# Kernel optimization log

Measured on AMD Instinct MI355X. Metric: run time of the kernel, lower is better.

## Reference

```python
import jax, jax.numpy as jnp
import numpy as np

B, D_ENC, T = 4, 512, 256
D_PRED, U = 640, 128
H, V = 640, 1025  # joint_hidden, num_classes + blank


def setup_inputs() -> dict:
    key = jax.random.key(0)
    ks = jax.random.split(key, 8)
    s = lambda d: 1.0 / np.sqrt(d)
    return {
        "encoder_outputs": jax.random.normal(ks[0], (B, D_ENC, T), jnp.float32),
        "decoder_outputs": jax.random.normal(ks[1], (B, D_PRED, U), jnp.float32),
        "W_enc": jax.random.normal(ks[2], (H, D_ENC), jnp.float32) * s(D_ENC),
        "b_enc": jax.random.normal(ks[3], (H,), jnp.float32) * s(D_ENC),
        "W_pred": jax.random.normal(ks[4], (H, D_PRED), jnp.float32) * s(D_PRED),
        "b_pred": jax.random.normal(ks[5], (H,), jnp.float32) * s(D_PRED),
        "W_out": jax.random.normal(ks[6], (V, H), jnp.float32) * s(H),
        "b_out": jax.random.normal(ks[7], (H,), jnp.float32)[:0],  # placeholder, replaced below
    } | {"b_out": jax.random.normal(jax.random.fold_in(key, 99), (V,), jnp.float32) * s(H)}


def reference(encoder_outputs, decoder_outputs, W_enc, b_enc, W_pred, b_pred, W_out, b_out):
    # transpose to (B, T, D_enc) and (B, U, D_pred)
    enc = jnp.swapaxes(encoder_outputs, 1, 2)
    dec = jnp.swapaxes(decoder_outputs, 1, 2)
    # projections to joint hidden
    f = jnp.einsum('bte,he->bth', enc, W_enc) + b_enc   # [B,T,H]
    g = jnp.einsum('bup,hp->buh', dec, W_pred) + b_pred  # [B,U,H]
    # broadcast add -> [B,T,U,H], ReLU, output linear, log-softmax
    h = jax.nn.relu(f[:, :, None, :] + g[:, None, :, :])
    logits = jnp.einsum('btuh,vh->btuv', h, W_out) + b_out  # [B,T,U,V]
    return jax.nn.log_softmax(logits, axis=-1)
```

## Files before the change

kernel.cpp:

```cpp
#include <hip/hip_runtime.h>
#include <hip/hip_bf16.h>

#define NB 4
#define NT 256
#define NU 128
#define DENC 512
#define DPRED 640
#define NH 640
#define NV 1025
#define NVP 1088
#define NTILES 68
#define JTA 8
#define JTB 9
#define JT 17
#define KSTEPS 20
#define WSLAB (NVP * 32)

typedef __attribute__((ext_vector_type(8))) short short8;
typedef __attribute__((ext_vector_type(4))) float f32x4;

__device__ __forceinline__ unsigned short bfu(float a) {
    union { __hip_bfloat16 h; unsigned short u; } cv;
    cv.h = __float2bfloat16(a);
    return cv.u;
}

__device__ __forceinline__ unsigned pk2(float a, float b) {
    union { __hip_bfloat162 h; unsigned u; } cv;
    cv.h = __float22bfloat162_rn(float2{a, b});
    return cv.u;
}

__device__ __forceinline__ short8 pack_relu(f32x4 x, f32x4 y) {
    union { short8 s; unsigned u[4]; } r;
    r.u[0] = pk2(fmaxf(x[0], 0.f), fmaxf(x[1], 0.f));
    r.u[1] = pk2(fmaxf(x[2], 0.f), fmaxf(x[3], 0.f));
    r.u[2] = pk2(fmaxf(y[0], 0.f), fmaxf(y[1], 0.f));
    r.u[3] = pk2(fmaxf(y[2], 0.f), fmaxf(y[3], 0.f));
    return r.s;
}

__device__ __forceinline__ void gload_lds16(const void* g, void* l) {
    __builtin_amdgcn_global_load_lds(
        (const __attribute__((address_space(1))) unsigned int*)g,
        (__attribute__((address_space(3))) unsigned int*)l, 16, 0, 0);
}

__global__ __launch_bounds__(256) void prep_kernel(const float* __restrict__ Wo,
                                                   const float* __restrict__ bo,
                                                   unsigned short* __restrict__ WbT,
                                                   float* __restrict__ biasp) {
    int idx = blockIdx.x * 256 + threadIdx.x;
    int ks = blockIdx.y;
    int r = idx >> 5;
    int kk = idx & 31;
    int s = kk >> 3, e = kk & 7;
    int f = ((r >> 2) ^ r) & 3;
    int scol = ks * 32 + (((s ^ f) & 3) << 3) + e;
    unsigned short val = 0;
    if (ks < KSTEPS && r < NV) val = bfu(Wo[r * NH + scol]);
    WbT[(size_t)ks * WSLAB + idx] = val;
    if (ks == 0 && idx < NVP) biasp[idx] = (idx < NV) ? bo[idx] : -1e30f;
}

__global__ __launch_bounds__(256) void proj_kernel(const float* __restrict__ X,
                                                   const float* __restrict__ W,
                                                   const float* __restrict__ bias,
                                                   float* __restrict__ out,
                                                   int L, int K) {
    __shared__ unsigned short As[32][40];
    __shared__ unsigned short Bs[64][40];
    int tid = threadIdx.x;
    int wave = tid >> 6, lane = tid & 63;
    int col16 = lane & 15, kgrp = lane >> 4;
    int m0 = blockIdx.x * 32;
    int n0 = blockIdx.y * 64;
    int b = m0 / L, l0 = m0 % L;
    const float* Xb = X + (size_t)b * K * L;

    float bv = bias[n0 + wave * 16 + col16];
    f32x4 c0 = {bv, bv, bv, bv};
    f32x4 c1 = c0;

    int ac = tid >> 3;
    int ar = (tid & 7) * 4;
    int bn = tid >> 2;
    int bc = (tid & 3) * 8;

    for (int k0 = 0; k0 < K; k0 += 32) {
        f32x4 av  = *(const f32x4*)(Xb + (size_t)(k0 + ac) * L + l0 + ar);
        f32x4 bw0 = *(const f32x4*)(W + (size_t)(n0 + bn) * K + k0 + bc);
        f32x4 bw1 = *(const f32x4*)(W + (size_t)(n0 + bn) * K + k0 + bc + 4);
        __syncthreads();
        As[ar + 0][ac] = bfu(av[0]);
        As[ar + 1][ac] = bfu(av[1]);
        As[ar + 2][ac] = bfu(av[2]);
        As[ar + 3][ac] = bfu(av[3]);
        unsigned* bsrow = (unsigned*)&Bs[bn][bc];
        bsrow[0] = pk2(bw0[0], bw0[1]);
        bsrow[1] = pk2(bw0[2], bw0[3]);
        bsrow[2] = pk2(bw1[0], bw1[1]);
        bsrow[3] = pk2(bw1[2], bw1[3]);
        __syncthreads();
        short8 a0  = *(const short8*)&As[col16][kgrp * 8];
        short8 a1  = *(const short8*)&As[16 + col16][kgrp * 8];
        short8 bfr = *(const short8*)&Bs[wave * 16 + col16][kgrp * 8];
        c0 = __builtin_amdgcn_mfma_f32_16x16x32_bf16(a0, bfr, c0, 0, 0, 0);
        c1 = __builtin_amdgcn_mfma_f32_16x16x32_bf16(a1, bfr, c1, 0, 0, 0);
    }
    int n = n0 + wave * 16 + col16;
    #pragma unroll
    for (int i = 0; i < 4; ++i) {
        int r0 = kgrp * 4 + i;
        out[(size_t)(m0 + r0) * NH + n]      = c0[i];
        out[(size_t)(m0 + 16 + r0) * NH + n] = c1[i];
    }
}

__global__ __launch_bounds__(256, 2) void joint_kernel(const float* __restrict__ f,
                                                       const float* __restrict__ g,
                                                       const unsigned short* __restrict__ WbT,
                                                       const float* __restrict__ biasp,
                                                       float* __restrict__ out) {
    __shared__ unsigned short Ws[WSLAB];
    __shared__ float fs[NH];
    __shared__ float redm[4][32];
    __shared__ float reds[4][32];
    int tid = threadIdx.x;
    int wave = tid >> 6, lane = tid & 63;
    int col16 = lane & 15, kgrp = lane >> 4;
    int bt = blockIdx.x >> 2;
    int u0 = (blockIdx.x & 3) * 32;
    int b = bt >> 8;

    for (int i = tid; i < NH; i += 256) fs[i] = f[(size_t)bt * NH + i];

    int tstart = wave * JT;
    unsigned short* WsA = &Ws[tstart * 512];
    unsigned short* WsB = &Ws[(tstart + JTA) * 512];

    const float* gp0 = g + (size_t)(b * NU + u0 + col16) * NH + kgrp * 8;
    const float* gp1 = gp0 + 16 * NH;

    f32x4 c[JT][2];
    #pragma unroll
    for (int j = 0; j < JT; ++j) {
        float bv = biasp[(tstart + j) * 16 + col16];
        f32x4 cv = {bv, bv, bv, bv};
        c[j][0] = cv; c[j][1] = cv;
    }

    int slx = ((kgrp ^ ((col16 >> 2) ^ col16)) & 3) * 8;
    int rdbase = col16 * 32 + slx;

    __syncthreads();

    f32x4 ga0 = *(const f32x4*)(gp0);
    f32x4 ga1 = *(const f32x4*)(gp0 + 4);
    f32x4 gb0 = *(const f32x4*)(gp1);
    f32x4 gb1 = *(const f32x4*)(gp1 + 4);
    #pragma unroll
    for (int jj = 0; jj < JTA; ++jj)
        gload_lds16(WbT + (size_t)(tstart + jj) * 512 + lane * 8, WsA + jj * 512);
    #pragma unroll
    for (int jj = 0; jj < JTB; ++jj)
        gload_lds16(WbT + (size_t)(tstart + JTA + jj) * 512 + lane * 8, WsB + jj * 512);

    for (int ks = 0; ks < KSTEPS; ++ks) {
        int kb = ks * 32 + kgrp * 8;
        f32x4 fa0 = *(const f32x4*)(fs + kb);
        f32x4 fa1 = *(const f32x4*)(fs + kb + 4);
        short8 a0 = pack_relu(fa0 + ga0, fa1 + ga1);
        short8 a1 = pack_relu(fa0 + gb0, fa1 + gb1);
        ga0 = *(const f32x4*)(gp0 + (ks + 1) * 32);
        ga1 = *(const f32x4*)(gp0 + (ks + 1) * 32 + 4);
        gb0 = *(const f32x4*)(gp1 + (ks + 1) * 32);
        gb1 = *(const f32x4*)(gp1 + (ks + 1) * 32 + 4);
        asm volatile("s_waitcnt vmcnt(13)" ::: "memory");
        __builtin_amdgcn_sched_barrier(0);
        __builtin_amdgcn_s_setprio(1);
        #pragma unroll
        for (int jj = 0; jj < JTA; ++jj) {
            short8 bj = *(const short8*)(WsA + jj * 512 + rdbase);
            c[jj][0] = __builtin_amdgcn_mfma_f32_16x16x32_bf16(a0, bj, c[jj][0], 0, 0, 0);
            c[jj][1] = __builtin_amdgcn_mfma_f32_16x16x32_bf16(a1, bj, c[jj][1], 0, 0, 0);
        }
        __builtin_amdgcn_s_setprio(0);
        asm volatile("s_waitcnt lgkmcnt(0)" ::: "memory");
        __builtin_amdgcn_sched_barrier(0);
        const unsigned short* wn = WbT + (size_t)(ks + 1) * WSLAB;
        #pragma unroll
        for (int jj = 0; jj < JTA; ++jj)
            gload_lds16(wn + (size_t)(tstart + jj) * 512 + lane * 8, WsA + jj * 512);
        asm volatile("s_waitcnt vmcnt(12)" ::: "memory");
        __builtin_amdgcn_sched_barrier(0);
        __builtin_amdgcn_s_setprio(1);
        #pragma unroll
        for (int jj = 0; jj < JTB; ++jj) {
            short8 bj = *(const short8*)(WsB + jj * 512 + rdbase);
            c[JTA + jj][0] = __builtin_amdgcn_mfma_f32_16x16x32_bf16(a0, bj, c[JTA + jj][0], 0, 0, 0);
            c[JTA + jj][1] = __builtin_amdgcn_mfma_f32_16x16x32_bf16(a1, bj, c[JTA + jj][1], 0, 0, 0);
        }
        __builtin_amdgcn_s_setprio(0);
        asm volatile("s_waitcnt lgkmcnt(0)" ::: "memory");
        __builtin_amdgcn_sched_barrier(0);
        #pragma unroll
        for (int jj = 0; jj < JTB; ++jj)
            gload_lds16(wn + (size_t)(tstart + JTA + jj) * 512 + lane * 8, WsB + jj * 512);
    }

    __syncthreads();

    float mx[2][4], sl[2][4];
    #pragma unroll
    for (int m = 0; m < 2; ++m) {
        #pragma unroll
        for (int i = 0; i < 4; ++i) {
            float v = -3e38f;
            #pragma unroll
            for (int j = 0; j < JT; ++j) v = fmaxf(v, c[j][m][i]);
            #pragma unroll
            for (int d = 1; d < 16; d <<= 1)
                v = fmaxf(v, __shfl_xor(v, d, 64));
            mx[m][i] = v;
        }
    }
    if (col16 == 0) {
        #pragma unroll
        for (int m = 0; m < 2; ++m)
            #pragma unroll
            for (int i = 0; i < 4; ++i)
                redm[wave][m * 16 + kgrp * 4 + i] = mx[m][i];
    }
    __syncthreads();
    #pragma unroll
    for (int m = 0; m < 2; ++m)
        #pragma unroll
        for (int i = 0; i < 4; ++i) {
            int r = m * 16 + kgrp * 4 + i;
            mx[m][i] = fmaxf(fmaxf(redm[0][r], redm[1][r]), fmaxf(redm[2][r], redm[3][r]));
        }
    #pragma unroll
    for (int m = 0; m < 2; ++m) {
        #pragma unroll
        for (int i = 0; i < 4; ++i) {
            float ssum = 0.f;
            #pragma unroll
            for (int j = 0; j < JT; ++j) ssum += __expf(c[j][m][i] - mx[m][i]);
            #pragma unroll
            for (int d = 1; d < 16; d <<= 1)
                ssum += __shfl_xor(ssum, d, 64);
            sl[m][i] = ssum;
        }
    }
    if (col16 == 0) {
        #pragma unroll
        for (int m = 0; m < 2; ++m)
            #pragma unroll
            for (int i = 0; i < 4; ++i)
                reds[wave][m * 16 + kgrp * 4 + i] = sl[m][i];
    }
    __syncthreads();
    #pragma unroll
    for (int m = 0; m < 2; ++m)
        #pragma unroll
        for (int i = 0; i < 4; ++i) {
            int r = m * 16 + kgrp * 4 + i;
            float S = (reds[0][r] + reds[1][r]) + (reds[2][r] + reds[3][r]);
            sl[m][i] = mx[m][i] + __logf(S);
        }

    size_t orow0 = (size_t)bt * NU + u0;
    #pragma unroll
    for (int m = 0; m < 2; ++m) {
        #pragma unroll
        for (int j = 0; j < JT; ++j) {
            int col = (tstart + j) * 16 + col16;
            if (col < NV) {
                #pragma unroll
                for (int i = 0; i < 4; ++i) {
                    size_t row = orow0 + m * 16 + kgrp * 4 + i;
                    out[row * (size_t)NV + col] = c[j][m][i] - sl[m][i];
                }
            }
        }
    }
}

extern "C" void kernel_launch(void* const* d_in, const int* in_sizes, int n_in,
                              void* d_out, int out_size, void* d_ws, size_t ws_size,
                              hipStream_t stream) {
    const float* enc    = (const float*)d_in[0];
    const float* dec    = (const float*)d_in[1];
    const float* W_enc  = (const float*)d_in[2];
    const float* b_enc  = (const float*)d_in[3];
    const float* W_pred = (const float*)d_in[4];
    const float* b_pred = (const float*)d_in[5];
    const float* W_out  = (const float*)d_in[6];
    const float* b_out  = (const float*)d_in[7];
    float* out = (float*)d_out;

    char* ws = (char*)d_ws;
    unsigned short* WbT = (unsigned short*)ws;
    float* biasp = (float*)(ws + 1462272);
    float* fbuf  = (float*)(ws + 1466624);
    float* gbuf  = (float*)(ws + 4088064);

    prep_kernel<<<dim3(WSLAB / 256, KSTEPS + 1), 256, 0, stream>>>(W_out, b_out, WbT, biasp);
    proj_kernel<<<dim3((NB * NT) / 32, NH / 64), 256, 0, stream>>>(enc, W_enc, b_enc, fbuf, NT, DENC);
    proj_kernel<<<dim3((NB * NU) / 32, NH / 64), 256, 0, stream>>>(dec, W_pred, b_pred, gbuf, NU, DPRED);
    joint_kernel<<<NB * NT * (NU / 32), 256, 0, stream>>>(fbuf, gbuf, WbT, biasp, out);
}
```

Baseline: 903.0 us.

## Share double-buffered W_out slab across two u-row wave groups in 512-thread blocks

```diff
diff --git a/kernel.cpp b/kernel.cpp
--- a/kernel.cpp
+++ b/kernel.cpp
@@ -10,8 +10,6 @@
 #define NV 1025
 #define NVP 1088
 #define NTILES 68
-#define JTA 8
-#define JTB 9
 #define JT 17
 #define KSTEPS 20
 #define WSLAB (NVP * 32)
@@ -117,29 +115,30 @@
     }
 }
 
-__global__ __launch_bounds__(256, 2) void joint_kernel(const float* __restrict__ f,
+__global__ __launch_bounds__(512, 2) void joint_kernel(const float* __restrict__ f,
                                                        const float* __restrict__ g,
                                                        const unsigned short* __restrict__ WbT,
                                                        const float* __restrict__ biasp,
                                                        float* __restrict__ out) {
-    __shared__ unsigned short Ws[WSLAB];
+    __shared__ unsigned short Ws[2][WSLAB];
     __shared__ float fs[NH];
-    __shared__ float redm[4][32];
-    __shared__ float reds[4][32];
+    __shared__ float redm[8][32];
+    __shared__ float reds[8][32];
     int tid = threadIdx.x;
     int wave = tid >> 6, lane = tid & 63;
+    int wm = wave >> 2, wn = wave & 3;
     int col16 = lane & 15, kgrp = lane >> 4;
-    int bt = blockIdx.x >> 2;
-    int u0 = (blockIdx.x & 3) * 32;
+    int bt = blockIdx.x >> 1;
+    int u0 = (blockIdx.x & 1) * 64;
     int b = bt >> 8;
 
-    for (int i = tid; i < NH; i += 256) fs[i] = f[(size_t)bt * NH + i];
-
-    int tstart = wave * JT;
-    unsigned short* WsA = &Ws[tstart * 512];
-    unsigned short* WsB = &Ws[(tstart + JTA) * 512];
-
-    const float* gp0 = g + (size_t)(b * NU + u0 + col16) * NH + kgrp * 8;
+    for (int i = tid; i < NH; i += 512) fs[i] = f[(size_t)bt * NH + i];
+
+    int tstart = wn * JT;
+    int sbase = tstart + (wm ? 9 : 0);
+    int scnt  = wm ? 8 : 9;
+
+    const float* gp0 = g + (size_t)(b * NU + u0 + wm * 32 + col16) * NH + kgrp * 8;
     const float* gp1 = gp0 + 16 * NH;
 
     f32x4 c[JT][2];
@@ -159,13 +158,11 @@
     f32x4 ga1 = *(const f32x4*)(gp0 + 4);
     f32x4 gb0 = *(const f32x4*)(gp1);
     f32x4 gb1 = *(const f32x4*)(gp1 + 4);
-    #pragma unroll
-    for (int jj = 0; jj < JTA; ++jj)
-        gload_lds16(WbT + (size_t)(tstart + jj) * 512 + lane * 8, WsA + jj * 512);
-    #pragma unroll
-    for (int jj = 0; jj < JTB; ++jj)
-        gload_lds16(WbT + (size_t)(tstart + JTA + jj) * 512 + lane * 8, WsB + jj * 512);
-
+    for (int jj = 0; jj < scnt; ++jj)
+        gload_lds16(WbT + (size_t)(sbase + jj) * 512 + lane * 8,
+                    &Ws[0][(sbase + jj) * 512]);
+
+    int cur = 0;
     for (int ks = 0; ks < KSTEPS; ++ks) {
         int kb = ks * 32 + kgrp * 8;
         f32x4 fa0 = *(const f32x4*)(fs + kb);
@@ -176,37 +173,29 @@
         ga1 = *(const f32x4*)(gp0 + (ks + 1) * 32 + 4);
         gb0 = *(const f32x4*)(gp1 + (ks + 1) * 32);
         gb1 = *(const f32x4*)(gp1 + (ks + 1) * 32 + 4);
-        asm volatile("s_waitcnt vmcnt(13)" ::: "memory");
+        {
+            const unsigned short* wnp = WbT + (size_t)(ks + 1) * WSLAB;
+            #pragma unroll
+            for (int jj = 0; jj < 9; ++jj)
+                if (jj < scnt)
+                    gload_lds16(wnp + (size_t)(sbase + jj) * 512 + lane * 8,
+                                &Ws[cur ^ 1][(sbase + jj) * 512]);
+        }
+        asm volatile("s_waitcnt vmcnt(12)" ::: "memory");
         __builtin_amdgcn_sched_barrier(0);
+        __builtin_amdgcn_s_barrier();
         __builtin_amdgcn_s_setprio(1);
         #pragma unroll
-        for (int jj = 0; jj < JTA; ++jj) {
-            short8 bj = *(const short8*)(WsA + jj * 512 + rdbase);
+        for (int jj = 0; jj < JT; ++jj) {
+            short8 bj = *(const short8*)(&Ws[cur][(tstart + jj) * 512 + rdbase]);
             c[jj][0] = __builtin_amdgcn_mfma_f32_16x16x32_bf16(a0, bj, c[jj][0], 0, 0, 0);
             c[jj][1] = __builtin_amdgcn_mfma_f32_16x16x32_bf16(a1, bj, c[jj][1], 0, 0, 0);
         }
         __builtin_amdgcn_s_setprio(0);
         asm volatile("s_waitcnt lgkmcnt(0)" ::: "memory");
         __builtin_amdgcn_sched_barrier(0);
-        const unsigned short* wn = WbT + (size_t)(ks + 1) * WSLAB;
-        #pragma unroll
-        for (int jj = 0; jj < JTA; ++jj)
-            gload_lds16(wn + (size_t)(tstart + jj) * 512 + lane * 8, WsA + jj * 512);
-        asm volatile("s_waitcnt vmcnt(12)" ::: "memory");
-        __builtin_amdgcn_sched_barrier(0);
-        __builtin_amdgcn_s_setprio(1);
-        #pragma unroll
-        for (int jj = 0; jj < JTB; ++jj) {
-            short8 bj = *(const short8*)(WsB + jj * 512 + rdbase);
-            c[JTA + jj][0] = __builtin_amdgcn_mfma_f32_16x16x32_bf16(a0, bj, c[JTA + jj][0], 0, 0, 0);
-            c[JTA + jj][1] = __builtin_amdgcn_mfma_f32_16x16x32_bf16(a1, bj, c[JTA + jj][1], 0, 0, 0);
-        }
-        __builtin_amdgcn_s_setprio(0);
-        asm volatile("s_waitcnt lgkmcnt(0)" ::: "memory");
-        __builtin_amdgcn_sched_barrier(0);
-        #pragma unroll
-        for (int jj = 0; jj < JTB; ++jj)
-            gload_lds16(wn + (size_t)(tstart + JTA + jj) * 512 + lane * 8, WsB + jj * 512);
+        __builtin_amdgcn_s_barrier();
+        cur ^= 1;
     }
 
     __syncthreads();
@@ -238,7 +227,9 @@
         #pragma unroll
         for (int i = 0; i < 4; ++i) {
             int r = m * 16 + kgrp * 4 + i;
-            mx[m][i] = fmaxf(fmaxf(redm[0][r], redm[1][r]), fmaxf(redm[2][r], redm[3][r]));
+            int wb = wm * 4;
+            mx[m][i] = fmaxf(fmaxf(redm[wb][r], redm[wb + 1][r]),
+                             fmaxf(redm[wb + 2][r], redm[wb + 3][r]));
         }
     #pragma unroll
     for (int m = 0; m < 2; ++m) {
@@ -266,11 +257,12 @@
         #pragma unroll
         for (int i = 0; i < 4; ++i) {
             int r = m * 16 + kgrp * 4 + i;
-            float S = (reds[0][r] + reds[1][r]) + (reds[2][r] + reds[3][r]);
+            int wb = wm * 4;
+            float S = (reds[wb][r] + reds[wb + 1][r]) + (reds[wb + 2][r] + reds[wb + 3][r]);
             sl[m][i] = mx[m][i] + __logf(S);
         }
 
-    size_t orow0 = (size_t)bt * NU + u0;
+    size_t orow0 = (size_t)bt * NU + u0 + wm * 32;
     #pragma unroll
     for (int m = 0; m < 2; ++m) {
         #pragma unroll
@@ -309,5 +301,5 @@
     prep_kernel<<<dim3(WSLAB / 256, KSTEPS + 1), 256, 0, stream>>>(W_out, b_out, WbT, biasp);
     proj_kernel<<<dim3((NB * NT) / 32, NH / 64), 256, 0, stream>>>(enc, W_enc, b_enc, fbuf, NT, DENC);
     proj_kernel<<<dim3((NB * NU) / 32, NH / 64), 256, 0, stream>>>(dec, W_pred, b_pred, gbuf, NU, DPRED);
-    joint_kernel<<<NB * NT * (NU / 32), 256, 0, stream>>>(fbuf, gbuf, WbT, biasp, out);
-}
+    joint_kernel<<<NB * NT * (NU / 64), 512, 0, stream>>>(fbuf, gbuf, WbT, biasp, out);
+}
```

Result: slower. 1.015 ms (+12.4%).
